# Kernel tuning notes

Hardware: AMD Instinct MI355X
Metric: run time of the kernel (lower is better)

The kernel has to match this reference:

```python
import jax, jax.numpy as jnp
import numpy as np

N = 300000      # total points
B = 4           # scenes
C_IN = 64
C_OUT = 128
GRID = 0.5      # voxel size
M = 128         # per-axis voxel index bound (10m / 0.5m = 20 << 128); key fits int32
EPS = 1e-5      # BatchNorm eps


def setup_inputs() -> dict:
    key = jax.random.key(0)
    k1, k2, k3 = jax.random.split(key, 3)
    coord = jax.random.uniform(k1, (N, 3), jnp.float32) * 10.0
    feat = jax.random.normal(k2, (N, C_IN), jnp.float32)
    offset = jnp.array([N // 4, N // 2, 3 * N // 4, N], jnp.int32)  # cumulative counts
    W = jax.random.normal(k3, (C_IN, C_OUT), jnp.float32) * 0.05    # fc weight (no bias)
    gamma = jnp.ones((C_OUT,), jnp.float32)
    beta = jnp.zeros((C_OUT,), jnp.float32)
    return {"coord": coord, "feat": feat, "offset": offset, "W": W, "gamma": gamma, "beta": beta}


def reference(coord, feat, offset, W, gamma, beta):
    n = coord.shape[0]
    # offset2batch: point i belongs to scene searchsorted(offset, i, 'right')
    batch = jnp.searchsorted(offset, jnp.arange(n, dtype=offset.dtype), side='right')
    # fc -> BatchNorm1d (training-mode batch stats, biased var) -> ReLU
    x = feat @ W                                    # [n, C_OUT]
    mean = x.mean(axis=0)
    var = x.var(axis=0)
    x = jax.nn.relu(gamma * (x - mean) * jax.lax.rsqrt(var + EPS) + beta)
    # start = per-scene min coordinate (segment_csr min)
    start = jax.ops.segment_min(coord, batch, num_segments=B)      # [B, 3]
    # voxel_grid: integer voxel index per point, hashed injectively with batch id
    v = jnp.floor((coord - start[batch]) / GRID).astype(jnp.int32)  # [n, 3]
    vkey = ((batch.astype(jnp.int32) * M + v[:, 0]) * M + v[:, 1]) * M + v[:, 2]
    # unique(sorted) with inverse/counts; padded to n for static shapes
    uniq, cluster, counts = jnp.unique(vkey, return_inverse=True, return_counts=True,
                                       size=n, fill_value=-1)
    cluster = cluster.reshape(-1)                   # [n] cluster id per point
    # segment mean of coords, segment max of features (padded segments -> 0)
    cnt = jnp.maximum(counts, 1).astype(coord.dtype)
    coord_out = jax.ops.segment_sum(coord, cluster, num_segments=n) / cnt[:, None]
    fmax = jax.ops.segment_max(x, cluster, num_segments=n)
    feat_out = jnp.where(counts[:, None] > 0, fmax, jnp.zeros((), x.dtype))
    # batch id of each cluster (clusters never cross scenes)
    batch_out = jax.ops.segment_min(batch, cluster, num_segments=n)
    return coord_out, feat_out, cluster, counts, batch_out
```

## Files before the change

kernel.cpp:

```cpp
#include <hip/hip_runtime.h>
#include <stdint.h>

#define CIN   64
#define COUT  128
#define EPSB  1e-5f
#define NWORDS2 4096
#define MAXNC 32768

typedef short bf16x8 __attribute__((ext_vector_type(8)));
typedef float f32x4  __attribute__((ext_vector_type(4)));
typedef unsigned u32x4 __attribute__((ext_vector_type(4)));

__device__ __forceinline__ int batch_of(int i, const int* __restrict__ off, int B) {
    int b = 0;
    for (int j = 0; j < B - 1; ++j) b += (i >= off[j]) ? 1 : 0;
    return b;
}

__device__ __forceinline__ unsigned enc(float x) {
    unsigned b = __float_as_uint(x);
    return (b & 0x80000000u) ? ~b : (b | 0x80000000u);
}
__device__ __forceinline__ float dec(unsigned u) {
    unsigned b = (u & 0x80000000u) ? (u ^ 0x80000000u) : ~u;
    return __uint_as_float(b);
}

__device__ __forceinline__ unsigned short rne_bf16(float f) {
    unsigned u = __float_as_uint(f);
    unsigned r = u + 0x7FFFu + ((u >> 16) & 1u);
    return (unsigned short)(r >> 16);
}

__device__ __forceinline__ void split8(float4 A, float4 B, bf16x8& hi, bf16x8& lo) {
    float fs[8] = {A.x, A.y, A.z, A.w, B.x, B.y, B.z, B.w};
    u32x4 hv, lv;
    #pragma unroll
    for (int w = 0; w < 4; ++w) {
        float a = fs[2*w], b = fs[2*w+1];
        unsigned ua = __float_as_uint(a), ub = __float_as_uint(b);
        hv[w] = __builtin_amdgcn_perm(ub, ua, 0x07060302u);
        float la = a - __uint_as_float(ua & 0xFFFF0000u);
        float lb = b - __uint_as_float(ub & 0xFFFF0000u);
        lv[w] = __builtin_amdgcn_perm(__float_as_uint(lb), __float_as_uint(la), 0x07060302u);
    }
    hi = __builtin_bit_cast(bf16x8, hv);
    lo = __builtin_bit_cast(bf16x8, lv);
}

__global__ void k_init(float* __restrict__ coordOut, float* __restrict__ batchOut, int n,
                       unsigned* __restrict__ pooledU, int* __restrict__ countsWs,
                       unsigned* __restrict__ flags, int* __restrict__ sceneMin, int nScene,
                       const float* __restrict__ W, unsigned short* __restrict__ Wb,
                       int* __restrict__ wCtr)
{
    long i = (long)blockIdx.x * blockDim.x + threadIdx.x;
    long stride = (long)gridDim.x * blockDim.x;
    if (i == 0) *wCtr = 0;
    for (long t = i; t < 3L * n; t += stride) coordOut[t] = 0.f;
    for (long t = i; t < n; t += stride) batchOut[t] = 2147483648.0f;
    for (long t = i; t < (long)MAXNC * COUT; t += stride) pooledU[t] = 0u;
    for (long t = i; t < MAXNC; t += stride) countsWs[t] = 0;
    for (long t = i; t < NWORDS2; t += stride) flags[t] = 0u;
    for (long t = i; t < nScene; t += stride) sceneMin[t] = 0x7F800000;
    for (long t = i; t < 32 * 64 * 8; t += stride) {
        int fragIdx = (int)(t >> 9);
        int r = (int)(t & 511);
        int lane = r >> 3, j = r & 7;
        int s  = fragIdx & 1;
        int kt = (fragIdx >> 1) & 1;
        int nt = fragIdx >> 2;
        int k  = kt * 32 + (lane >> 4) * 8 + j;
        int nc = nt * 16 + (lane & 15);
        float w = W[k * COUT + nc];
        unsigned short hi = rne_bf16(w);
        if (s == 0) Wb[t] = hi;
        else {
            float hf = __uint_as_float(((unsigned)hi) << 16);
            Wb[t] = rne_bf16(w - hf);
        }
    }
}

__global__ void k_scene_min(const float* __restrict__ coord, const int* __restrict__ off,
                            int n, int B, int* __restrict__ sceneMin)
{
    __shared__ int smin[12];
    if (threadIdx.x < 3 * B) smin[threadIdx.x] = 0x7F800000;
    __syncthreads();
    int t = blockIdx.x * blockDim.x + threadIdx.x;
    if (t < n) {
        int b = batch_of(t, off, B);
        for (int d = 0; d < 3; ++d)
            atomicMin(&smin[b * 3 + d], __float_as_int(coord[t * 3 + d]));
    }
    __syncthreads();
    if (threadIdx.x < 3 * B) atomicMin(&sceneMin[threadIdx.x], smin[threadIdx.x]);
}

__global__ void k_vkey(const float* __restrict__ coord, const int* __restrict__ off,
                       int n, int B, const int* __restrict__ sceneMin,
                       int* __restrict__ vkeyWs, unsigned* __restrict__ flags)
{
    int t = blockIdx.x * blockDim.x + threadIdx.x;
    if (t >= n) return;
    int b = batch_of(t, off, B);
    int key = b;
    #pragma unroll
    for (int d = 0; d < 3; ++d) {
        float s = __int_as_float(sceneMin[b * 3 + d]);
        int v = (int)floorf((coord[t * 3 + d] - s) * 2.0f);
        key = (key << 5) + v;
    }
    vkeyWs[t] = key;
    atomicOr(&flags[key >> 5], 1u << (key & 31));
}

__global__ void k_scan1(const unsigned* __restrict__ flags,
                        unsigned* __restrict__ wordPrefix, int* __restrict__ dNC)
{
    __shared__ unsigned wsum[16];
    const int t = threadIdx.x, lane = t & 63, wv = t >> 6;
    unsigned loc[4]; unsigned sum = 0;
    #pragma unroll
    for (int e = 0; e < 4; ++e) { loc[e] = (unsigned)__popc(flags[4 * t + e]); sum += loc[e]; }
    unsigned incl = sum;
    #pragma unroll
    for (int d = 1; d < 64; d <<= 1) {
        unsigned u = __shfl_up(incl, d, 64);
        if (lane >= d) incl += u;
    }
    if (lane == 63) wsum[wv] = incl;
    __syncthreads();
    if (wv == 0) {
        unsigned v = (lane < 16) ? wsum[lane] : 0u;
        unsigned iv = v;
        #pragma unroll
        for (int d = 1; d < 16; d <<= 1) {
            unsigned u = __shfl_up(iv, d, 64);
            if (lane >= d) iv += u;
        }
        if (lane < 16) wsum[lane] = iv - v;
    }
    __syncthreads();
    unsigned run = wsum[wv] + incl - sum;
    #pragma unroll
    for (int e = 0; e < 4; ++e) { wordPrefix[4 * t + e] = run; run += loc[e]; }
    if (t == 1023) *dNC = (int)run;
}

__global__ void k_cluster(const int* __restrict__ vkeyWs, const int* __restrict__ off,
                          int n, int B,
                          const unsigned* __restrict__ flags, const unsigned* __restrict__ wordPrefix,
                          float* __restrict__ clusterOut,
                          int* __restrict__ countsWs, float* __restrict__ batchOut)
{
    int t = blockIdx.x * blockDim.x + threadIdx.x;
    if (t >= n) return;
    int key = vkeyWs[t];
    int w = key >> 5, bit = key & 31;
    int c = (int)wordPrefix[w] + __popc(flags[w] & ((1u << bit) - 1u));
    clusterOut[t] = (float)c;
    atomicAdd(&countsWs[c], 1);
    batchOut[c] = (float)(key >> 15);
}

__global__ void k_scan2(const int* __restrict__ counts, int* __restrict__ cursor)
{
    __shared__ int wsum[16];
    const int t = threadIdx.x, lane = t & 63, wv = t >> 6;
    const int base = t * 32;
    int loc[32]; int sum = 0;
    #pragma unroll
    for (int e = 0; e < 32; ++e) { loc[e] = counts[base + e]; sum += loc[e]; }
    int incl = sum;
    #pragma unroll
    for (int d = 1; d < 64; d <<= 1) {
        int u = __shfl_up(incl, d, 64);
        if (lane >= d) incl += u;
    }
    if (lane == 63) wsum[wv] = incl;
    __syncthreads();
    if (wv == 0) {
        int v = (lane < 16) ? wsum[lane] : 0;
        int iv = v;
        #pragma unroll
        for (int d = 1; d < 16; d <<= 1) {
            int u = __shfl_up(iv, d, 64);
            if (lane >= d) iv += u;
        }
        if (lane < 16) wsum[lane] = iv - v;
    }
    __syncthreads();
    int run = wsum[wv] + incl - sum;
    #pragma unroll
    for (int e = 0; e < 32; ++e) { cursor[base + e] = run; run += loc[e]; }
}

__global__ void k_scatter(const float* __restrict__ clusterOut, int n,
                          int* __restrict__ cursor, int2* __restrict__ pcPair)
{
    int t = blockIdx.x * blockDim.x + threadIdx.x;
    if (t >= n) return;
    int c = (int)clusterOut[t];
    int pos = atomicAdd(&cursor[c], 1);
    pcPair[pos] = make_int2(t, c);
}

template<bool FULL>
__device__ __forceinline__ void do_window(
    int wid, int n, const float* __restrict__ feat, const float* __restrict__ coord,
    const unsigned short* __restrict__ Wb, const int2* __restrict__ pc,
    unsigned* __restrict__ pooledU, float* __restrict__ coordOut,
    float* __restrict__ accS, float* __restrict__ slab, int lane)
{
    const int q = lane >> 4, c16 = lane & 15;
    const int base = wid * 64;
    const int nvalid = FULL ? 64 : (n - base);

    int pv = 0, cv = -1;
    if (FULL || lane < nvalid) { int2 t = pc[base + lane]; pv = t.x; cv = t.y; }
    int prevc = __shfl_up(cv, 1, 64);
    unsigned long long bmask = __ballot(lane > 0 && (FULL || lane < nvalid) && cv != prevc);

    {
        float cx = 0.f, cy = 0.f, cz = 0.f;
        if (FULL || lane < nvalid) {
            const float* cp = coord + 3 * (size_t)pv;
            cx = cp[0]; cy = cp[1]; cz = cp[2];
        }
        unsigned long long mlow = bmask & (~0ull >> (63 - lane));
        int rs = mlow ? (63 - __clzll((long long)mlow)) : 0;
        #pragma unroll
        for (int d = 1; d < 64; d <<= 1) {
            float tx = __shfl_up(cx, d, 64);
            float ty = __shfl_up(cy, d, 64);
            float tz = __shfl_up(cz, d, 64);
            if (lane - rs >= d) { cx += tx; cy += ty; cz += tz; }
        }
        bool isEnd = (lane == nvalid - 1) || ((((bmask >> 1) >> lane) & 1ull) != 0ull);
        if ((FULL || lane < nvalid) && isEnd) {
            float* cb = coordOut + (size_t)cv * 3;
            if (rs == 0 || lane == nvalid - 1) {
                atomicAdd(cb + 0, cx); atomicAdd(cb + 1, cy); atomicAdd(cb + 2, cz);
            } else {
                cb[0] = cx; cb[1] = cy; cb[2] = cz;
            }
        }
    }

    const int rk = (lane >> 3) & 3;
    int rdOff[4], wOff[4];
    #pragma unroll
    for (int g = 0; g < 4; ++g) rdOff[g] = lane * 16 + (((g ^ rk) & 3) << 2);
    #pragma unroll
    for (int t2 = 0; t2 < 4; ++t2) {
        int col = t2 * 16 + c16;
        wOff[t2] = col * 16 + (((q ^ ((col >> 3) & 3)) & 3) << 2);
    }

    const unsigned short* wb = Wb + (lane << 3);

    #pragma unroll 1
    for (int h = 0; h < 2; ++h) {
        bf16x8 bh[4][2], bl[4][2];
        #pragma unroll
        for (int nt2 = 0; nt2 < 4; ++nt2)
            #pragma unroll
            for (int kt = 0; kt < 2; ++kt) {
                int fi = h * 16 + (nt2 * 2 + kt) * 2;
                bh[nt2][kt] = *(const bf16x8*)(wb + ((size_t)fi << 9));
                bl[nt2][kt] = *(const bf16x8*)(wb + ((size_t)(fi + 1) << 9));
            }
        float runM = -__builtin_inff(), s1 = 0.f, s2 = 0.f;
        int runStart = 0;
        #pragma unroll 1
        for (int mt = 0; mt < 4; ++mt) {
            int m = mt * 16 + c16;
            int p = __shfl(pv, m, 64);
            const float* ap = feat + (size_t)p * CIN + q * 8;
            bf16x8 ahi[2], alo[2];
            #pragma unroll
            for (int kt = 0; kt < 2; ++kt) {
                float4 fa = make_float4(0.f, 0.f, 0.f, 0.f), fb = fa;
                if (FULL || m < nvalid) {
                    fa = *(const float4*)(ap + kt * 32);
                    fb = *(const float4*)(ap + kt * 32 + 4);
                }
                split8(fa, fb, ahi[kt], alo[kt]);
            }
            #pragma unroll
            for (int t2 = 0; t2 < 4; ++t2) {
                f32x4 c = {0.f, 0.f, 0.f, 0.f};
                c = __builtin_amdgcn_mfma_f32_16x16x32_bf16(alo[0], bh[t2][0], c, 0, 0, 0);
                c = __builtin_amdgcn_mfma_f32_16x16x32_bf16(ahi[0], bl[t2][0], c, 0, 0, 0);
                c = __builtin_amdgcn_mfma_f32_16x16x32_bf16(ahi[0], bh[t2][0], c, 0, 0, 0);
                c = __builtin_amdgcn_mfma_f32_16x16x32_bf16(alo[1], bh[t2][1], c, 0, 0, 0);
                c = __builtin_amdgcn_mfma_f32_16x16x32_bf16(ahi[1], bl[t2][1], c, 0, 0, 0);
                c = __builtin_amdgcn_mfma_f32_16x16x32_bf16(ahi[1], bh[t2][1], c, 0, 0, 0);
                *(float4*)&slab[wOff[t2]] = make_float4(c[0], c[1], c[2], c[3]);
            }
            #pragma unroll
            for (int g = 0; g < 4; ++g) {
                float4 v = *(const float4*)&slab[rdOff[g]];
                #pragma unroll
                for (int e = 0; e < 4; ++e) {
                    const int i = mt * 16 + g * 4 + e;
                    if (i > 0 && ((bmask >> i) & 1ull)) {
                        int pcid = __shfl(cv, i - 1, 64);
                        unsigned* pb = pooledU + (size_t)pcid * COUT + h * 64 + lane;
                        if (runStart == 0) atomicMax(pb, enc(runM));
                        else               *pb = enc(runM);
                        runStart = i;
                        runM = -__builtin_inff();
                    }
                    float x = (e == 0) ? v.x : (e == 1) ? v.y : (e == 2) ? v.z : v.w;
                    if (FULL || i < nvalid) runM = fmaxf(runM, x);
                    s1 += x;
                    s2 = fmaf(x, x, s2);
                }
            }
        }
        int cidL = __shfl(cv, nvalid - 1, 64);
        atomicMax(pooledU + (size_t)cidL * COUT + h * 64 + lane, enc(runM));
        atomicAdd(&accS[h * 64 + lane],       s1);
        atomicAdd(&accS[128 + h * 64 + lane], s2);
    }
}

__global__ __launch_bounds__(256, 3) void k_fused(
    const float* __restrict__ feat, const float* __restrict__ coord,
    const unsigned short* __restrict__ Wb, const int2* __restrict__ pc,
    int n, int nWin, int gFused, int* __restrict__ wCtr,
    unsigned* __restrict__ pooledU, float* __restrict__ coordOut,
    float* __restrict__ partials)
{
    __shared__ float slabs[4][64 * 16];
    __shared__ float accS[256];
    const int tid = threadIdx.x, wave = tid >> 6, lane = tid & 63;
    accS[tid] = 0.f;
    __syncthreads();
    float* slab = slabs[wave];

    for (;;) {
        int w = 0;
        if (lane == 0) w = atomicAdd(wCtr, 1);
        w = __shfl(w, 0, 64);
        if (w >= nWin) break;
        if (w < nWin - 1)
            do_window<true >(w, n, feat, coord, Wb, pc, pooledU, coordOut, accS, slab, lane);
        else
            do_window<false>(w, n, feat, coord, Wb, pc, pooledU, coordOut, accS, slab, lane);
    }

    __syncthreads();
    partials[(size_t)tid * gFused + blockIdx.x] = accS[tid];
}

__global__ void k_redbn(const float* __restrict__ partials, int gFused,
                        const float* __restrict__ gamma, const float* __restrict__ beta,
                        int n, float* __restrict__ scaleShift)
{
    __shared__ float red[512];
    const int j = blockIdx.x;
    const float* colS = partials + (size_t)j * gFused;
    const float* colQ = partials + (size_t)(j + 128) * gFused;
    float s = 0.f, q = 0.f;
    for (int b = threadIdx.x; b < gFused; b += 256) { s += colS[b]; q += colQ[b]; }
    red[threadIdx.x] = s;
    red[256 + threadIdx.x] = q;
    __syncthreads();
    for (int st = 128; st; st >>= 1) {
        if (threadIdx.x < st) {
            red[threadIdx.x] += red[threadIdx.x + st];
            red[256 + threadIdx.x] += red[256 + threadIdx.x + st];
        }
        __syncthreads();
    }
    if (threadIdx.x == 0) {
        float mean = red[0] / (float)n;
        float var  = red[256] / (float)n - mean * mean;
        var = fmaxf(var, 0.f);
        float inv = rsqrtf(var + EPSB);
        float sc = gamma[j] * inv;
        scaleShift[j]        = sc;
        scaleShift[COUT + j] = beta[j] - mean * sc;
    }
}

__global__ void k_final(float* __restrict__ featOut, const unsigned* __restrict__ pooledU,
                        const int* __restrict__ dNC, const float* __restrict__ scaleShift,
                        long featN4, int n,
                        float* __restrict__ coordOut, float* __restrict__ countsOut,
                        const int* __restrict__ countsWs)
{
    long i = (long)blockIdx.x * blockDim.x + threadIdx.x;
    long stride = (long)gridDim.x * blockDim.x;
    long act4 = (long)(*dNC) * (COUT / 4);
    float4* out4 = (float4*)featOut;
    const uint4* p4 = (const uint4*)pooledU;
    for (long idx = i; idx < featN4; idx += stride) {
        float4 v = make_float4(0.f, 0.f, 0.f, 0.f);
        if (idx < act4) {
            int j = (int)((idx * 4) & (COUT - 1));
            uint4 u = p4[idx];
            v.x = fmaxf(fmaf(scaleShift[j + 0], dec(u.x), scaleShift[COUT + j + 0]), 0.f);
            v.y = fmaxf(fmaf(scaleShift[j + 1], dec(u.y), scaleShift[COUT + j + 1]), 0.f);
            v.z = fmaxf(fmaf(scaleShift[j + 2], dec(u.z), scaleShift[COUT + j + 2]), 0.f);
            v.w = fmaxf(fmaf(scaleShift[j + 3], dec(u.w), scaleShift[COUT + j + 3]), 0.f);
        }
        out4[idx] = v;
    }
    for (long t = i; t < n; t += stride) {
        int cnt = (t < MAXNC) ? countsWs[t] : 0;
        if (cnt > 0) {
            float inv = 1.f / (float)cnt;
            coordOut[3 * t + 0] *= inv;
            coordOut[3 * t + 1] *= inv;
            coordOut[3 * t + 2] *= inv;
        }
        countsOut[t] = (float)cnt;
    }
}

extern "C" void kernel_launch(void* const* d_in, const int* in_sizes, int n_in,
                              void* d_out, int out_size, void* d_ws, size_t ws_size,
                              hipStream_t stream)
{
    const float* coord = (const float*)d_in[0];
    const float* feat  = (const float*)d_in[1];
    const int*   off   = (const int*)d_in[2];
    const float* W     = (const float*)d_in[3];
    const float* gamma = (const float*)d_in[4];
    const float* beta  = (const float*)d_in[5];
    const int n = in_sizes[0] / 3;
    const int B = in_sizes[2];

    float* out        = (float*)d_out;
    float* coordOut   = out;
    float* featOut    = out + (long)n * 3;
    float* clusterOut = featOut + (long)n * COUT;
    float* countsOut  = clusterOut + n;
    float* batchOut   = countsOut + n;

    char* wsp = (char*)d_ws;
    auto alloc = [&](size_t bytes) -> char* {
        char* p = wsp;
        wsp += (bytes + 255) & ~(size_t)255;
        return p;
    };
    unsigned* flags      = (unsigned*)alloc(NWORDS2 * 4);
    unsigned* wordPrefix = (unsigned*)alloc(NWORDS2 * 4);
    int*      vkeyWs     = (int*)alloc((size_t)n * 4);
    int*      countsWs   = (int*)alloc(MAXNC * 4);
    int2*     pcPair     = (int2*)alloc((size_t)n * sizeof(int2));
    int*      cursor     = (int*)alloc(MAXNC * 4);
    unsigned* pooledU    = (unsigned*)alloc((size_t)MAXNC * COUT * 4);
    unsigned short* Wb   = (unsigned short*)alloc(32 * 64 * 8 * 2);
    float*    scaleShift = (float*)alloc(2 * COUT * 4);
    int*      sceneMin   = (int*)alloc(3 * B * 4);
    int*      dNC        = (int*)alloc(4);
    int*      wCtr       = (int*)alloc(4);

    const int nWin = (n + 63) / 64;
    const int gFused = 1024;
    float*    partials   = (float*)alloc((size_t)gFused * 256 * 4);

    const long featN4 = (long)n * COUT / 4;
    const int nb = (n + 255) / 256;

    k_init<<<nb, 256, 0, stream>>>(coordOut, batchOut, n, pooledU, countsWs,
                                   flags, sceneMin, 3 * B, W, Wb, wCtr);
    k_scene_min<<<nb, 256, 0, stream>>>(coord, off, n, B, sceneMin);
    k_vkey<<<nb, 256, 0, stream>>>(coord, off, n, B, sceneMin, vkeyWs, flags);
    k_scan1<<<1, 1024, 0, stream>>>(flags, wordPrefix, dNC);
    k_cluster<<<nb, 256, 0, stream>>>(vkeyWs, off, n, B, flags, wordPrefix,
                                      clusterOut, countsWs, batchOut);
    k_scan2<<<1, 1024, 0, stream>>>(countsWs, cursor);
    k_scatter<<<nb, 256, 0, stream>>>(clusterOut, n, cursor, pcPair);
    k_fused<<<gFused, 256, 0, stream>>>(feat, coord, Wb, pcPair, n, nWin, gFused, wCtr,
                                        pooledU, coordOut, partials);
    k_redbn<<<128, 256, 0, stream>>>(partials, gFused, gamma, beta, n, scaleShift);
    k_final<<<2048, 256, 0, stream>>>(featOut, pooledU, dNC, scaleShift, featN4, n,
                                      coordOut, countsOut, countsWs);
}
```

Measured before the change: 437.8 us.

## Preload and split window features once, reuse across halves, pad LDS slab

All feature rows for a 64-point window are now loaded into registers at the start of the window and split into bf16 hi/lo once. Before, they were reloaded and re-split in each of the two output-channel halves. Issuing these loads before the coordinate prefix scan should overlap their latency with that work, and the m-tile loop is now fully unrolled. The XOR-swizzled LDS slab is replaced by a stride-17 padded layout. That layout makes the float4 LDS accesses misaligned, and the held A fragments raise register pressure under the 3-blocks-per-SM launch bound.

```diff
diff --git a/kernel.cpp b/kernel.cpp
--- a/kernel.cpp
+++ b/kernel.cpp
@@ -6,6 +6,7 @@
 #define EPSB  1e-5f
 #define NWORDS2 4096
 #define MAXNC 32768
+#define SLABW 17
 
 typedef short bf16x8 __attribute__((ext_vector_type(8)));
 typedef float f32x4  __attribute__((ext_vector_type(4)));
@@ -223,12 +224,28 @@
     int prevc = __shfl_up(cv, 1, 64);
     unsigned long long bmask = __ballot(lane > 0 && (FULL || lane < nvalid) && cv != prevc);
 
+    float cx = 0.f, cy = 0.f, cz = 0.f;
+    if (FULL || lane < nvalid) {
+        const float* cp = coord + 3 * (size_t)pv;
+        cx = cp[0]; cy = cp[1]; cz = cp[2];
+    }
+
+    int pmt[4];
+    #pragma unroll
+    for (int mt = 0; mt < 4; ++mt) pmt[mt] = __shfl(pv, mt * 16 + c16, 64);
+    float4 Ar[4][2][2];
+    #pragma unroll
+    for (int mt = 0; mt < 4; ++mt) {
+        const bool ok = FULL || (mt * 16 + c16 < nvalid);
+        const float* ap = feat + (size_t)pmt[mt] * CIN + q * 8;
+        #pragma unroll
+        for (int kt = 0; kt < 2; ++kt) {
+            Ar[mt][kt][0] = ok ? *(const float4*)(ap + kt * 32)     : make_float4(0.f,0.f,0.f,0.f);
+            Ar[mt][kt][1] = ok ? *(const float4*)(ap + kt * 32 + 4) : make_float4(0.f,0.f,0.f,0.f);
+        }
+    }
+
     {
-        float cx = 0.f, cy = 0.f, cz = 0.f;
-        if (FULL || lane < nvalid) {
-            const float* cp = coord + 3 * (size_t)pv;
-            cx = cp[0]; cy = cp[1]; cz = cp[2];
-        }
         unsigned long long mlow = bmask & (~0ull >> (63 - lane));
         int rs = mlow ? (63 - __clzll((long long)mlow)) : 0;
         #pragma unroll
@@ -249,15 +266,18 @@
         }
     }
 
-    const int rk = (lane >> 3) & 3;
+    bf16x8 ahi[4][2], alo[4][2];
+    #pragma unroll
+    for (int mt = 0; mt < 4; ++mt)
+        #pragma unroll
+        for (int kt = 0; kt < 2; ++kt)
+            split8(Ar[mt][kt][0], Ar[mt][kt][1], ahi[mt][kt], alo[mt][kt]);
+
     int rdOff[4], wOff[4];
     #pragma unroll
-    for (int g = 0; g < 4; ++g) rdOff[g] = lane * 16 + (((g ^ rk) & 3) << 2);
-    #pragma unroll
-    for (int t2 = 0; t2 < 4; ++t2) {
-        int col = t2 * 16 + c16;
-        wOff[t2] = col * 16 + (((q ^ ((col >> 3) & 3)) & 3) << 2);
-    }
+    for (int g = 0; g < 4; ++g) rdOff[g] = lane * SLABW + g * 4;
+    #pragma unroll
+    for (int t2 = 0; t2 < 4; ++t2) wOff[t2] = (t2 * 16 + c16) * SLABW + q * 4;
 
     const unsigned short* wb = Wb + (lane << 3);
 
@@ -274,30 +294,17 @@
             }
         float runM = -__builtin_inff(), s1 = 0.f, s2 = 0.f;
         int runStart = 0;
-        #pragma unroll 1
+        #pragma unroll
         for (int mt = 0; mt < 4; ++mt) {
-            int m = mt * 16 + c16;
-            int p = __shfl(pv, m, 64);
-            const float* ap = feat + (size_t)p * CIN + q * 8;
-            bf16x8 ahi[2], alo[2];
-            #pragma unroll
-            for (int kt = 0; kt < 2; ++kt) {
-                float4 fa = make_float4(0.f, 0.f, 0.f, 0.f), fb = fa;
-                if (FULL || m < nvalid) {
-                    fa = *(const float4*)(ap + kt * 32);
-                    fb = *(const float4*)(ap + kt * 32 + 4);
-                }
-                split8(fa, fb, ahi[kt], alo[kt]);
-            }
             #pragma unroll
             for (int t2 = 0; t2 < 4; ++t2) {
                 f32x4 c = {0.f, 0.f, 0.f, 0.f};
-                c = __builtin_amdgcn_mfma_f32_16x16x32_bf16(alo[0], bh[t2][0], c, 0, 0, 0);
-                c = __builtin_amdgcn_mfma_f32_16x16x32_bf16(ahi[0], bl[t2][0], c, 0, 0, 0);
-                c = __builtin_amdgcn_mfma_f32_16x16x32_bf16(ahi[0], bh[t2][0], c, 0, 0, 0);
-                c = __builtin_amdgcn_mfma_f32_16x16x32_bf16(alo[1], bh[t2][1], c, 0, 0, 0);
-                c = __builtin_amdgcn_mfma_f32_16x16x32_bf16(ahi[1], bl[t2][1], c, 0, 0, 0);
-                c = __builtin_amdgcn_mfma_f32_16x16x32_bf16(ahi[1], bh[t2][1], c, 0, 0, 0);
+                c = __builtin_amdgcn_mfma_f32_16x16x32_bf16(alo[mt][0], bh[t2][0], c, 0, 0, 0);
+                c = __builtin_amdgcn_mfma_f32_16x16x32_bf16(ahi[mt][0], bl[t2][0], c, 0, 0, 0);
+                c = __builtin_amdgcn_mfma_f32_16x16x32_bf16(ahi[mt][0], bh[t2][0], c, 0, 0, 0);
+                c = __builtin_amdgcn_mfma_f32_16x16x32_bf16(alo[mt][1], bh[t2][1], c, 0, 0, 0);
+                c = __builtin_amdgcn_mfma_f32_16x16x32_bf16(ahi[mt][1], bl[t2][1], c, 0, 0, 0);
+                c = __builtin_amdgcn_mfma_f32_16x16x32_bf16(ahi[mt][1], bh[t2][1], c, 0, 0, 0);
                 *(float4*)&slab[wOff[t2]] = make_float4(c[0], c[1], c[2], c[3]);
             }
             #pragma unroll
@@ -335,7 +342,7 @@
     unsigned* __restrict__ pooledU, float* __restrict__ coordOut,
     float* __restrict__ partials)
 {
-    __shared__ float slabs[4][64 * 16];
+    __shared__ float slabs[4][64 * SLABW];
     __shared__ float accS[256];
     const int tid = threadIdx.x, wave = tid >> 6, lane = tid & 63;
     accS[tid] = 0.f;
```

Measured after the change: 456.4 us. 4.3% more time.
